# Kernel tuning notes

Measured on AMD Instinct MI355X. Metric: run time of the kernel, lower is better.

Reference implementation:

```python
import jax, jax.numpy as jnp
import numpy as np

DOWNSAMPLE_RATE = 4
DISCRETE_RATIO = 0.4  # voxel_size[0]


def setup_inputs() -> dict:
    key = jax.random.key(0)
    B, N, C, H, W = 4, 4, 64, 128, 256
    L = 5
    k1, k2 = jax.random.split(key)
    x = jax.random.normal(k1, (B * N, C, H, W), jnp.float32)
    # near-identity transforms so the warp is a realistic small affine perturbation
    noise = jax.random.normal(k2, (B, L, L, 4, 4), jnp.float32) * 0.05
    pairwise_t_matrix = jnp.eye(4, dtype=jnp.float32)[None, None, None] + noise
    record_len = jnp.full((B,), N, jnp.int32)
    return {"x": x, "pairwise_t_matrix": pairwise_t_matrix, "record_len": record_len}


def _warp_affine_simple(img, M, H, W):
    """torch affine_grid + grid_sample (bilinear, zeros padding, align_corners=True).
    img: (C, H, W); M: (2, 3) normalized affine matrix."""
    xs = jnp.linspace(-1.0, 1.0, W, dtype=img.dtype)
    ys = jnp.linspace(-1.0, 1.0, H, dtype=img.dtype)
    gy, gx = jnp.meshgrid(ys, xs, indexing="ij")           # (H, W)
    base = jnp.stack([gx, gy, jnp.ones_like(gx)], axis=-1)  # (H, W, 3)
    g = base @ M.T                                          # (H, W, 2) -> (x, y) in [-1, 1]
    ix = (g[..., 0] + 1.0) * 0.5 * (W - 1)
    iy = (g[..., 1] + 1.0) * 0.5 * (H - 1)
    x0 = jnp.floor(ix).astype(jnp.int32)
    y0 = jnp.floor(iy).astype(jnp.int32)
    x1, y1 = x0 + 1, y0 + 1
    wx = (ix - x0).astype(img.dtype)
    wy = (iy - y0).astype(img.dtype)

    def gather(yi, xi):
        valid = ((xi >= 0) & (xi < W) & (yi >= 0) & (yi < H)).astype(img.dtype)
        v = img[:, jnp.clip(yi, 0, H - 1), jnp.clip(xi, 0, W - 1)]  # (C, H, W)
        return v * valid

    return (gather(y0, x0) * ((1 - wx) * (1 - wy))
            + gather(y0, x1) * (wx * (1 - wy))
            + gather(y1, x0) * ((1 - wx) * wy)
            + gather(y1, x1) * (wx * wy))


def reference(x, pairwise_t_matrix, record_len):
    _, C, H, W = x.shape
    B, L = pairwise_t_matrix.shape[:2]
    N = x.shape[0] // B  # record_len is constant N per batch here

    # pairwise_t_matrix[:, :, :, [0,1], :][:, :, :, :, [0,1,3]]
    tm = pairwise_t_matrix[:, :, :, :2, :][..., jnp.array([0, 1, 3])]  # (B, L, L, 2, 3)
    tm = tm.at[..., 0, 1].multiply(H / W)
    tm = tm.at[..., 1, 0].multiply(W / H)
    tm = tm.at[..., 0, 2].set(tm[..., 0, 2] / (DOWNSAMPLE_RATE * DISCRETE_RATIO * W) * 2)
    tm = tm.at[..., 1, 2].set(tm[..., 1, 2] / (DOWNSAMPLE_RATE * DISCRETE_RATIO * H) * 2)

    # regroup: (B*N, C, H, W) -> (B, N, C, H, W)
    feats = x.reshape(B, N, C, H, W)
    M = tm[:, 0, :N]  # (B, N, 2, 3): transform from each cav to ego

    warp = jax.vmap(jax.vmap(_warp_affine_simple, in_axes=(0, 0, None, None)),
                    in_axes=(0, 0, None, None))
    neighbor = warp(feats, M, H, W)  # (B, N, C, H, W)

    # AttenFusion: per-pixel attention over cav dim, keep only ego (index 0) output
    f = neighbor.reshape(B, N, C, H * W).transpose(0, 3, 1, 2)  # (B, P, N, C)
    scale = 1.0 / np.sqrt(C)
    q0 = f[:, :, 0, :]                                   # (B, P, C) ego query
    score = jnp.einsum("bpc,bpmc->bpm", q0, f) * scale   # (B, P, N)
    attn = jax.nn.softmax(score, axis=-1)
    ctx = jnp.einsum("bpm,bpmc->bpc", attn, f)           # (B, P, C)
    x_fuse = ctx.transpose(0, 2, 1).reshape(B, C, H, W)
    return x_fuse
```

## Files before the change

### kernel.cpp

```cpp
#include <hip/hip_runtime.h>
#include <math.h>

namespace {
constexpr int B = 4, N = 4, C = 64, H = 128, W = 256, L = 5;
constexpr int HW = H * W;
constexpr int WAVES = 8;
constexpr int CPW = C / WAVES;
constexpr int NXCD = 8;
constexpr int NWG = B * (W / 64) * H;
}

typedef float f2v __attribute__((ext_vector_type(2), aligned(4)));

__global__ __launch_bounds__(512, 4) void atten_comm_kernel(
    const float* __restrict__ x,
    const float* __restrict__ P,
    float* __restrict__ out)
{
    __shared__ float sred[WAVES][N][64];

    const int g    = (int)blockIdx.x;
    const int orig = (g & (NXCD - 1)) * (NWG / NXCD) + (g >> 3);
    const int h    = orig & (H - 1);
    const int wc   = (orig >> 7) & 3;
    const int b    = orig >> 9;

    const int lane = (int)(threadIdx.x & 63);
    const int wv   = (int)(threadIdx.x >> 6);
    const int w    = (wc << 6) + lane;

    const float gx = -1.0f + (2.0f / (float)(W - 1)) * (float)w;
    const float gy = -1.0f + (2.0f / (float)(H - 1)) * (float)h;

    const float* basep[N];
    int   voff0[N], voff1[N];
    float u0x[N], u0y[N], u1x[N], u1y[N];

#pragma unroll
    for (int n = 0; n < N; ++n) {
        const float* p = P + ((size_t)b * L * L + (size_t)n) * 16;
        const float a  = p[0];
        const float bb = p[1] * ((float)H / (float)W);
        const float cc = p[3] * (2.0f / (4.0f * 0.4f * (float)W));
        const float d  = p[4] * ((float)W / (float)H);
        const float e  = p[5];
        const float ff = p[7] * (2.0f / (4.0f * 0.4f * (float)H));

        const float g0 = a * gx + bb * gy + cc;
        const float g1 = d * gx + e * gy + ff;
        const float ix = (g0 + 1.0f) * (0.5f * (float)(W - 1));
        const float iy = (g1 + 1.0f) * (0.5f * (float)(H - 1));

        const float fx0 = floorf(ix);
        const float fy0 = floorf(iy);
        const int x0 = (int)fx0, y0 = (int)fy0;
        const int y1 = y0 + 1;
        const float wx = ix - fx0;
        const float wy = iy - fy0;

        const int   xa   = min(max(x0, 0), W - 2);
        const float wx0v = (1.0f - wx) * ((x0 >= 0 && x0 < W) ? 1.0f : 0.0f);
        const float wx1v = wx * ((x0 + 1 >= 0 && x0 + 1 < W) ? 1.0f : 0.0f);
        const float ux = (x0 < 0) ? wx1v : ((x0 > W - 2) ? 0.0f : wx0v);
        const float uy = (x0 < 0) ? 0.0f : ((x0 > W - 2) ? wx0v : wx1v);

        const int yc0 = min(max(y0, 0), H - 1);
        const int yc1 = min(max(y1, 0), H - 1);
        const float wyv0 = (1.0f - wy) * ((y0 >= 0 && y0 < H) ? 1.0f : 0.0f);
        const float wyv1 = wy * ((y1 >= 0 && y1 < H) ? 1.0f : 0.0f);

        u0x[n] = ux * wyv0;  u0y[n] = uy * wyv0;
        u1x[n] = ux * wyv1;  u1y[n] = uy * wyv1;
        voff0[n] = yc0 * W + xa;
        voff1[n] = yc1 * W + xa;

        basep[n] = x + ((size_t)(b * N + n) * C + (size_t)(wv * CPW)) * HW;
    }

    float f[N][CPW];
#pragma unroll
    for (int cc = 0; cc < CPW; ++cc) {
        f2v t0[N], t1[N];
#pragma unroll
        for (int n = 0; n < N; ++n) {
            const float* pl = basep[n] + (size_t)cc * HW;
            t0[n] = *(const f2v*)(pl + voff0[n]);
            t1[n] = *(const f2v*)(pl + voff1[n]);
        }
#pragma unroll
        for (int n = 0; n < N; ++n) {
            f[n][cc] = u0x[n] * t0[n].x + u0y[n] * t0[n].y
                     + u1x[n] * t1[n].x + u1y[n] * t1[n].y;
        }
    }

    float s[N] = {0.f, 0.f, 0.f, 0.f};
#pragma unroll
    for (int cc = 0; cc < CPW; ++cc) {
        const float q = f[0][cc];
#pragma unroll
        for (int n = 0; n < N; ++n) s[n] += q * f[n][cc];
    }

#pragma unroll
    for (int n = 0; n < N; ++n) sred[wv][n][lane] = s[n];
    __syncthreads();

    float st[N];
#pragma unroll
    for (int n = 0; n < N; ++n) {
        float acc = 0.f;
#pragma unroll
        for (int v = 0; v < WAVES; ++v) acc += sred[v][n][lane];
        st[n] = acc;
    }

    const float scale = 0.125f;
    const float s0 = st[0] * scale, s1 = st[1] * scale;
    const float s2 = st[2] * scale, s3 = st[3] * scale;
    const float m  = fmaxf(fmaxf(s0, s1), fmaxf(s2, s3));
    const float e0 = expf(s0 - m);
    const float e1 = expf(s1 - m);
    const float e2 = expf(s2 - m);
    const float e3 = expf(s3 - m);
    const float inv = 1.0f / (e0 + e1 + e2 + e3);
    const float attn[N] = {e0 * inv, e1 * inv, e2 * inv, e3 * inv};

    float* op = out + ((size_t)b * C + (size_t)(wv * CPW)) * HW
                    + (size_t)h * W + (size_t)w;
#pragma unroll
    for (int cc = 0; cc < CPW; ++cc) {
        float ctx = 0.f;
#pragma unroll
        for (int n = 0; n < N; ++n) ctx += attn[n] * f[n][cc];
        op[(size_t)cc * HW] = ctx;
    }
}

extern "C" void kernel_launch(void* const* d_in, const int* in_sizes, int n_in,
                              void* d_out, int out_size, void* d_ws, size_t ws_size,
                              hipStream_t stream) {
    const float* x  = (const float*)d_in[0];
    const float* P  = (const float*)d_in[1];
    float* out = (float*)d_out;

    dim3 block(512, 1, 1);
    dim3 grid(NWG, 1, 1);
    hipLaunchKernelGGL(atten_comm_kernel, grid, block, 0, stream, x, P, out);
}
```

Before: 45.62 us.

## Split channels across two workgroups per pixel row and recompute scores redundantly

Doubles the grid so each workgroup handles half the channels (4 per wave instead of 8), lowering per-thread register use and raising occupancy/parallelism. Because the attention score needs a dot product over all channels, each workgroup also gathers and interpolates the other half of the channels just to compute partial scores, then adds them in shared memory. This trades roughly 1.5x the gather traffic and interpolation work for smaller per-block live state and more blocks in flight.

```diff
diff --git a/kernel.cpp b/kernel.cpp
--- a/kernel.cpp
+++ b/kernel.cpp
@@ -5,9 +5,9 @@
 constexpr int B = 4, N = 4, C = 64, H = 128, W = 256, L = 5;
 constexpr int HW = H * W;
 constexpr int WAVES = 8;
-constexpr int CPW = C / WAVES;
+constexpr int CPW = 4;
 constexpr int NXCD = 8;
-constexpr int NWG = B * (W / 64) * H;
+constexpr int NWG = B * (W / 64) * H * 2;
 }
 
 typedef float f2v __attribute__((ext_vector_type(2), aligned(4)));
@@ -19,15 +19,17 @@
 {
     __shared__ float sred[WAVES][N][64];
 
-    const int g    = (int)blockIdx.x;
-    const int orig = (g & (NXCD - 1)) * (NWG / NXCD) + (g >> 3);
-    const int h    = orig & (H - 1);
-    const int wc   = (orig >> 7) & 3;
-    const int b    = orig >> 9;
+    const int g     = (int)blockIdx.x;
+    const int orig  = (g & (NXCD - 1)) * (NWG / NXCD) + (g >> 3);
+    const int chalf = orig & 1;
+    const int h     = (orig >> 1) & (H - 1);
+    const int wc    = (orig >> 8) & 3;
+    const int b     = orig >> 10;
 
     const int lane = (int)(threadIdx.x & 63);
     const int wv   = (int)(threadIdx.x >> 6);
     const int w    = (wc << 6) + lane;
+    const int cbase = chalf * (C / 2) + wv * CPW;
 
     const float gx = -1.0f + (2.0f / (float)(W - 1)) * (float)w;
     const float gy = -1.0f + (2.0f / (float)(H - 1)) * (float)h;
@@ -74,7 +76,7 @@
         voff0[n] = yc0 * W + xa;
         voff1[n] = yc1 * W + xa;
 
-        basep[n] = x + ((size_t)(b * N + n) * C + (size_t)(wv * CPW)) * HW;
+        basep[n] = x + ((size_t)(b * N + n) * C + (size_t)cbase) * HW;
     }
 
     float f[N][CPW];
@@ -104,6 +106,35 @@
 
 #pragma unroll
     for (int n = 0; n < N; ++n) sred[wv][n][lane] = s[n];
+
+    {
+        const int sbase = cbase ^ (C / 2);
+        float s2[N] = {0.f, 0.f, 0.f, 0.f};
+#pragma unroll
+        for (int cc = 0; cc < CPW; ++cc) {
+            f2v t0[N], t1[N];
+#pragma unroll
+            for (int n = 0; n < N; ++n) {
+                const float* pl = basep[n] + ((size_t)(sbase - cbase) + (size_t)cc) * HW;
+                t0[n] = *(const f2v*)(pl + voff0[n]);
+                t1[n] = *(const f2v*)(pl + voff1[n]);
+            }
+            float fv[N];
+#pragma unroll
+            for (int n = 0; n < N; ++n) {
+                fv[n] = u0x[n] * t0[n].x + u0y[n] * t0[n].y
+                      + u1x[n] * t1[n].x + u1y[n] * t1[n].y;
+            }
+            const float q = fv[0];
+#pragma unroll
+            for (int n = 0; n < N; ++n) s2[n] += q * fv[n];
+        }
+        __syncthreads();
+#pragma unroll
+        for (int n = 0; n < N; ++n) {
+            sred[wv][n][lane] += s2[n];
+        }
+    }
     __syncthreads();
 
     float st[N];
@@ -126,7 +157,7 @@
     const float inv = 1.0f / (e0 + e1 + e2 + e3);
     const float attn[N] = {e0 * inv, e1 * inv, e2 * inv, e3 * inv};
 
-    float* op = out + ((size_t)b * C + (size_t)(wv * CPW)) * HW
+    float* op = out + ((size_t)b * C + (size_t)cbase) * HW
                     + (size_t)h * W + (size_t)w;
 #pragma unroll
     for (int cc = 0; cc < CPW; ++cc) {
```

New measurement: 76.19 us. 67.0% more time.
